# Kernel optimization log

Measured on AMD Instinct MI355X. Metric: run time of the kernel, lower is better.

Reference implementation:

```python
import jax, jax.numpy as jnp
from jax import lax
import numpy as np

EPS = 1e-07


def _sum_pool3_same(x):
    """TF avg_pool2d(3,1,'SAME')*9: sum over 3x3 window, edge windows scaled by 9/valid_count."""
    # x: [b, h, w, q]
    window = (1, 3, 3, 1)
    strides = (1, 1, 1, 1)
    s = lax.reduce_window(x, 0.0, lax.add, window, strides, 'SAME')
    ones = jnp.ones((1, x.shape[1], x.shape[2], 1), dtype=x.dtype)
    cnt = lax.reduce_window(ones, 0.0, lax.add, window, strides, 'SAME')
    return s / cnt * 9.0


def setup_inputs() -> dict:
    key = jax.random.key(0)
    k1, k2 = jax.random.split(key)
    foreground = jax.random.normal(k1, (4, 64, 64, 256), dtype=jnp.float32)
    masks = jax.random.uniform(k2, (4, 256, 256, 1), dtype=jnp.float32)
    return {"foreground": foreground, "masks": masks}


def reference(foreground, masks):
    # foreground: [bz, h, w, nc]; first-call forward (att_scores_prev is None).
    bz, h, w, nc = foreground.shape
    # masks resized to feature resolution (stored as state in original; no effect on output)
    if masks.shape[1] != h:
        masks = jax.image.resize(masks, (bz, h, w, masks.shape[-1]), method='bilinear')

    # 1x1 dynamic conv kernels from the feature map itself: K[b, q, c], q = flattened (h*w)
    K = (foreground + EPS).reshape(bz, h * w, nc)
    norm = jnp.sqrt(jnp.sum(K * K, axis=-1, keepdims=True))  # L2 norm per output channel q
    K = K / norm

    # conv2d with 1x1 kernels == per-pixel inner product with every patch center
    scores = jnp.einsum('bijc,bqc->bijq', foreground, K)  # [bz, h, w, h*w]

    # propagate_size=3: 3x3 smoothing (avg_pool * 9, TF edge-count semantics)
    scores = _sum_pool3_same(scores)

    att = jax.nn.softmax(scores, axis=-1)  # softmax over the h*w patch axis

    # conv2d_transpose with the same 1x1 kernels == weighted sum of patch features
    out = jnp.einsum('bijq,bqc->bijc', att, K)  # [bz, h, w, nc]
    return out
```

## Files before the change

### kernel.cpp

```cpp
#include <hip/hip_runtime.h>


#define EPSV 1e-7f

typedef __bf16 bf16x8 __attribute__((ext_vector_type(8)));
typedef float f32x4 __attribute__((ext_vector_type(4)));
typedef unsigned short ushort8v __attribute__((ext_vector_type(8)));

__device__ __forceinline__ unsigned short f2bf(float f) {
    union { float f; unsigned int u; } x; x.f = f;
    unsigned int r = x.u + 0x7FFFu + ((x.u >> 16) & 1u);
    return (unsigned short)(r >> 16);
}

__device__ __forceinline__ f32x4 mfma16(bf16x8 a, bf16x8 b, f32x4 c) {
    return __builtin_amdgcn_mfma_f32_16x16x32_bf16(a, b, c, 0, 0, 0);
}

__device__ __forceinline__ void gload_lds16(const void* g, void* l) {
    __builtin_amdgcn_global_load_lds((const __attribute__((address_space(1))) void*)g,
                                     (__attribute__((address_space(3))) void*)l, 16, 0, 0);
}

__global__ __launch_bounds__(256) void prep_kv(const float* __restrict__ F,
                                               unsigned short* __restrict__ Khi2,
                                               unsigned short* __restrict__ Vt2) {
    __shared__ unsigned short ldsT[256 * 74];
    __shared__ unsigned short ldsR[64 * 264];
    const int tid = threadIdx.x;
    const int w = tid >> 6, lane = tid & 63;
    const int q0 = blockIdx.x * 64;
    const int b = blockIdx.y;
    const size_t bq = (size_t)b * 4096;

    for (int r = 0; r < 16; ++r) {
        const int qloc = w * 16 + r;
        const int q = q0 + qloc;
        const float4 f = *(const float4*)(F + ((bq + q) << 8) + lane * 4);
        float v0 = f.x + EPSV, v1 = f.y + EPSV, v2 = f.z + EPSV, v3 = f.w + EPSV;
        float ss = v0 * v0 + v1 * v1 + v2 * v2 + v3 * v3;
        #pragma unroll
        for (int m = 1; m <= 32; m <<= 1) ss += __shfl_xor(ss, m);
        const float inv = 1.0f / sqrtf(ss);
        const unsigned short k0 = f2bf(v0 * inv), k1 = f2bf(v1 * inv);
        const unsigned short k2 = f2bf(v2 * inv), k3 = f2bf(v3 * inv);
        ushort4 kk; kk.x = k0; kk.y = k1; kk.z = k2; kk.w = k3;
        *(ushort4*)(ldsR + qloc * 264 + lane * 4) = kk;
        ldsT[(lane * 4 + 0) * 74 + qloc] = k0;
        ldsT[(lane * 4 + 1) * 74 + qloc] = k1;
        ldsT[(lane * 4 + 2) * 74 + qloc] = k2;
        ldsT[(lane * 4 + 3) * 74 + qloc] = k3;
    }
    __syncthreads();

    const size_t tbase = (size_t)b * 128 + (size_t)blockIdx.x * 2;

    #pragma unroll
    for (int tsub = 0; tsub < 2; ++tsub) {
        char* dstK = (char*)Khi2 + ((tbase + tsub) << 14);
        #pragma unroll
        for (int i = 0; i < 4; ++i) {
            const int fi = i * 256 + tid;
            const int chunk = fi >> 6, L = fi & 63;
            const int l15 = L & 15, g4v = L >> 4;
            const int kg = chunk >> 1, ct = chunk & 1;
            const int qloc = tsub * 32 + ct * 16 + l15;
            const int c0 = kg * 32 + g4v * 8;
            *(ushort8v*)(dstK + fi * 16) = *(const ushort8v*)(ldsR + qloc * 264 + c0);
        }
    }

    const int c = tid;
    const int c16v = c >> 4, l15c = c & 15;
    const unsigned short* row = ldsT + c * 74;
    #pragma unroll
    for (int tsub = 0; tsub < 2; ++tsub) {
        const unsigned short* qrow = row + tsub * 32;
        #pragma unroll
        for (int g4v = 0; g4v < 4; ++g4v) {
            ushort8v frag;
            #pragma unroll
            for (int e = 0; e < 8; ++e)
                frag[e] = qrow[(g4v * 4 + (e >> 1)) + ((e & 1) << 4)];
            *(ushort8v*)((char*)Vt2 + ((tbase + tsub) << 14) + (c16v << 10) +
                         ((g4v * 16 + l15c) << 4)) = frag;
        }
    }
}

__global__ __launch_bounds__(256) void prep_g(const float* __restrict__ F,
                                              unsigned short* __restrict__ G) {
    __shared__ float vs[64 * 256];
    const int tid = threadIdx.x;
    const int i = blockIdx.x, b = blockIdx.y;
    const size_t bq = (size_t)b * 4096;
    const int i0 = i > 0 ? i - 1 : 0, i1 = i < 63 ? i + 1 : 63;
    #pragma unroll
    for (int k2 = 0; k2 < 16; ++k2) {
        const int cell = k2 * 256 + tid;
        const int j = cell >> 6, c4 = (cell & 63) << 2;
        float4 acc = {0.f, 0.f, 0.f, 0.f};
        for (int ii = i0; ii <= i1; ++ii) {
            const float4 f = *(const float4*)(F + ((bq + ii * 64 + j) << 8) + c4);
            acc.x += f.x; acc.y += f.y; acc.z += f.z; acc.w += f.w;
        }
        *(float4*)(vs + j * 256 + c4) = acc;
    }
    __syncthreads();
    const float ri = (float)(i1 - i0 + 1);
    #pragma unroll
    for (int k2 = 0; k2 < 16; ++k2) {
        const int cell = k2 * 256 + tid;
        const int j = cell >> 6, c4 = (cell & 63) << 2;
        const int j0 = j > 0 ? j - 1 : 0, j1 = j < 63 ? j + 1 : 63;
        float4 s = {0.f, 0.f, 0.f, 0.f};
        for (int jj = j0; jj <= j1; ++jj) {
            const float4 v = *(const float4*)(vs + jj * 256 + c4);
            s.x += v.x; s.y += v.y; s.z += v.z; s.w += v.w;
        }
        const float scale = 9.0f / (ri * (float)(j1 - j0 + 1));
        ushort4 gv; gv.x = f2bf(s.x * scale); gv.y = f2bf(s.y * scale);
        gv.z = f2bf(s.z * scale); gv.w = f2bf(s.w * scale);
        *(ushort4*)(G + ((bq + i * 64 + j) << 8) + c4) = gv;
    }
}

template <int ATOMIC>
__global__ __launch_bounds__(256, 2) void attn_main(
        const unsigned short* __restrict__ Khi2, const unsigned short* __restrict__ Vt2,
        const unsigned short* __restrict__ G, float* __restrict__ wsl,
        float* __restrict__ dOut, float* __restrict__ wsO) {
    __shared__ unsigned short ldsK[2][32 * 256];
    __shared__ unsigned short ldsV[2][32 * 256];
    __shared__ unsigned int ldsP[4][32 * 20];
    const int tid = threadIdx.x;
    const int w = tid >> 6, lane = tid & 63;
    const int l15 = lane & 15, g4 = lane >> 4;

    const int bid = blockIdx.x;
    const int u = bid & 7, v = bid >> 3;
    const int group = u * 2 + (v >> 5);
    const int pb = v & 31;
    const int split = group >> 2, b = group & 3;

    const int pw = pb * 128 + w * 32;
    const size_t bq = (size_t)b * 4096;

    const char* KhiB = (const char*)Khi2 + (((size_t)b * 128 + split * 32) << 14);
    const char* VtB = (const char*)Vt2 + (((size_t)b * 128 + split * 32) << 14);

    #pragma unroll
    for (int it = 0; it < 4; ++it) {
        const int g = it * 256 + tid;
        gload_lds16(KhiB + g * 16, (char*)&ldsK[0][0] + g * 16);
    }
    #pragma unroll
    for (int it = 0; it < 4; ++it) {
        const int g = it * 256 + tid;
        gload_lds16(VtB + g * 16, (char*)&ldsV[0][0] + g * 16);
    }

    bf16x8 a[2][8];
    #pragma unroll
    for (int rt = 0; rt < 2; ++rt)
        #pragma unroll
        for (int kg = 0; kg < 8; ++kg)
            a[rt][kg] = *(const bf16x8*)(G + ((bq + pw + rt * 16 + l15) << 8) + (kg << 5) + (g4 << 3));

    f32x4 o[2][16];
    float lacc[2][4];
    #pragma unroll
    for (int rt = 0; rt < 2; ++rt) {
        #pragma unroll
        for (int c16 = 0; c16 < 16; ++c16) o[rt][c16] = f32x4{0.f, 0.f, 0.f, 0.f};
        #pragma unroll
        for (int r = 0; r < 4; ++r) lacc[rt][r] = 0.f;
    }
    unsigned int* Pw = &ldsP[w][0];

    __syncthreads();

    #pragma unroll 1
    for (int t = 0; t < 32; ++t) {
        const int cur = t & 1;

        if (t < 31) {
            const char* ks = KhiB + ((size_t)(t + 1) << 14);
            #pragma unroll
            for (int it = 0; it < 4; ++it) {
                const int g = it * 256 + tid;
                gload_lds16(ks + g * 16, (char*)&ldsK[cur ^ 1][0] + g * 16);
            }
            const char* vs2 = VtB + ((size_t)(t + 1) << 14);
            #pragma unroll
            for (int it = 0; it < 4; ++it) {
                const int g = it * 256 + tid;
                gload_lds16(vs2 + g * 16, (char*)&ldsV[cur ^ 1][0] + g * 16);
            }
        }

        f32x4 s[2][2];
        #pragma unroll
        for (int rt = 0; rt < 2; ++rt) {
            s[rt][0] = f32x4{0.f, 0.f, 0.f, 0.f};
            s[rt][1] = f32x4{0.f, 0.f, 0.f, 0.f};
        }
        const char* kb = (const char*)&ldsK[cur][0] + (lane << 4);
        __builtin_amdgcn_s_setprio(1);
        #pragma unroll
        for (int kg = 0; kg < 8; ++kg) {
            #pragma unroll
            for (int ct = 0; ct < 2; ++ct) {
                const bf16x8 bk = *(const bf16x8*)(kb + (kg * 2 + ct) * 1024);
                s[0][ct] = mfma16(a[0][kg], bk, s[0][ct]);
                s[1][ct] = mfma16(a[1][kg], bk, s[1][ct]);
            }
        }
        __builtin_amdgcn_s_setprio(0);

        bf16x8 a2[2];
        #pragma unroll
        for (int rt = 0; rt < 2; ++rt) {
            #pragma unroll
            for (int r = 0; r < 4; ++r) {
                const float e0 = __expf(s[rt][0][r]);
                const float e1 = __expf(s[rt][1][r]);
                lacc[rt][r] += e0 + e1;
                union { __bf16 h[2]; unsigned int u; } pk;
                pk.h[0] = (__bf16)e0; pk.h[1] = (__bf16)e1;
                Pw[(rt * 16 + g4 * 4 + r) * 20 + l15] = pk.u;
            }
            a2[rt] = *(const bf16x8*)((const char*)Pw + (rt * 16 + l15) * 80 + (g4 << 4));
        }

        const char* vbase = (const char*)&ldsV[cur][0] + (lane << 4);
        __builtin_amdgcn_s_setprio(1);
        #pragma unroll
        for (int c16 = 0; c16 < 16; ++c16) {
            const bf16x8 bv = *(const bf16x8*)(vbase + c16 * 1024);
            o[0][c16] = mfma16(bv, a2[0], o[0][c16]);
            o[1][c16] = mfma16(bv, a2[1], o[1][c16]);
        }
        __builtin_amdgcn_s_setprio(0);

        if (t < 31) __syncthreads();
    }

    #pragma unroll
    for (int rt = 0; rt < 2; ++rt)
        #pragma unroll
        for (int r = 0; r < 4; ++r) {
            float vsum = lacc[rt][r];
            #pragma unroll
            for (int m = 1; m <= 8; m <<= 1) vsum += __shfl_xor(vsum, m);
            lacc[rt][r] = vsum;
        }
    if (l15 == 0) {
        #pragma unroll
        for (int rt = 0; rt < 2; ++rt)
            #pragma unroll
            for (int r = 0; r < 4; ++r)
                wsl[(size_t)split * 16384 + bq + pw + rt * 16 + g4 * 4 + r] = lacc[rt][r];
    }

    if (!ATOMIC) {
        float* dst = (split == 0) ? dOut : (wsO + (size_t)(split - 1) * 4194304);
        #pragma unroll
        for (int rt = 0; rt < 2; ++rt)
            #pragma unroll
            for (int c16 = 0; c16 < 16; ++c16)
                *(f32x4*)(dst + ((bq + pw + rt * 16 + l15) << 8) + c16 * 16 + (g4 << 2)) = o[rt][c16];
    } else {
        #pragma unroll
        for (int rt = 0; rt < 2; ++rt)
            #pragma unroll
            for (int c16 = 0; c16 < 16; ++c16)
                #pragma unroll
                for (int r = 0; r < 4; ++r) {
                    const size_t idx = ((bq + pw + rt * 16 + l15) << 8) + c16 * 16 + (g4 << 2) + r;
                    atomicAdd(&dOut[idx], o[rt][c16][r]);
                }
    }
}

__global__ __launch_bounds__(256) void reduce_fin(float* __restrict__ dOut,
                                                  const float* __restrict__ wsO,
                                                  const float* __restrict__ wsl) {
    const int i4 = blockIdx.x * 256 + threadIdx.x;
    const int row = i4 >> 6;
    const float l = wsl[row] + wsl[16384 + row] + wsl[32768 + row] + wsl[49152 + row];
    const float inv = 1.0f / l;
    float4 v = ((const float4*)dOut)[i4];
    const float4 a = ((const float4*)wsO)[i4];
    const float4 b = ((const float4*)(wsO + 4194304))[i4];
    const float4 c = ((const float4*)(wsO + 8388608))[i4];
    v.x = (v.x + a.x + b.x + c.x) * inv;
    v.y = (v.y + a.y + b.y + c.y) * inv;
    v.z = (v.z + a.z + b.z + c.z) * inv;
    v.w = (v.w + a.w + b.w + c.w) * inv;
    ((float4*)dOut)[i4] = v;
}

__global__ __launch_bounds__(256) void divide_fin(float* __restrict__ dOut,
                                                  const float* __restrict__ wsl) {
    const int i4 = blockIdx.x * 256 + threadIdx.x;
    const int row = i4 >> 6;
    const float l = wsl[row] + wsl[16384 + row] + wsl[32768 + row] + wsl[49152 + row];
    const float inv = 1.0f / l;
    float4 v = ((const float4*)dOut)[i4];
    v.x *= inv; v.y *= inv; v.z *= inv; v.w *= inv;
    ((float4*)dOut)[i4] = v;
}

extern "C" void kernel_launch(void* const* d_in, const int* in_sizes, int n_in,
                              void* d_out, int out_size, void* d_ws, size_t ws_size,
                              hipStream_t stream) {
    const float* F = (const float*)d_in[0];
    float* out = (float*)d_out;
    char* ws = (char*)d_ws;

    unsigned short* Khi2 = (unsigned short*)ws;
    unsigned short* Vt2 = Khi2 + 4194304;
    unsigned short* G = Vt2 + 4194304;
    float* wsl = (float*)(ws + 25165824);
    float* wsO = (float*)(ws + 25165824 + 262144);
    const size_t needA = 25165824u + 262144u + 3u * 16777216u;

    prep_kv<<<dim3(64, 4), 256, 0, stream>>>(F, Khi2, Vt2);
    prep_g<<<dim3(64, 4), 256, 0, stream>>>(F, G);

    if (ws_size >= needA) {
        attn_main<0><<<dim3(512), 256, 0, stream>>>(Khi2, Vt2, G, wsl, out, wsO);
        reduce_fin<<<4096, 256, 0, stream>>>(out, wsO, wsl);
    } else {
        hipMemsetAsync(out, 0, 16777216, stream);
        attn_main<1><<<dim3(512), 256, 0, stream>>>(Khi2, Vt2, G, wsl, out, nullptr);
        divide_fin<<<4096, 256, 0, stream>>>(out, wsl);
    }
}
```

Before: 126.0 us.

## Restructure attention kernel to 512-thread blocks with 64-key tiles and shared P

The attention kernel now uses 8 waves per block and processes 64-key tiles instead of 32. Each wave computes scores for 64 rows against a 16-key slice and writes exp values to a swizzled shared P buffer. For the PV product, each wave covers a 64-channel slice across all keys, so V fragments are reused over four row tiles. The softmax denominator is now computed with an MFMA against a ones vector rather than shuffle reductions. Prep_kv writes the K/V images in the new 64-key tile layout, and an extra block-wide barrier per tile is added to share P.

```diff
diff --git a/kernel.cpp b/kernel.cpp
--- a/kernel.cpp
+++ b/kernel.cpp
@@ -23,8 +23,8 @@
 }
 
 __global__ __launch_bounds__(256) void prep_kv(const float* __restrict__ F,
-                                               unsigned short* __restrict__ Khi2,
-                                               unsigned short* __restrict__ Vt2) {
+                                               unsigned short* __restrict__ Kimg,
+                                               unsigned short* __restrict__ Vimg) {
     __shared__ unsigned short ldsT[256 * 74];
     __shared__ unsigned short ldsR[64 * 264];
     const int tid = threadIdx.x;
@@ -53,39 +53,31 @@
     }
     __syncthreads();
 
-    const size_t tbase = (size_t)b * 128 + (size_t)blockIdx.x * 2;
-
-    #pragma unroll
-    for (int tsub = 0; tsub < 2; ++tsub) {
-        char* dstK = (char*)Khi2 + ((tbase + tsub) << 14);
-        #pragma unroll
-        for (int i = 0; i < 4; ++i) {
-            const int fi = i * 256 + tid;
-            const int chunk = fi >> 6, L = fi & 63;
-            const int l15 = L & 15, g4v = L >> 4;
-            const int kg = chunk >> 1, ct = chunk & 1;
-            const int qloc = tsub * 32 + ct * 16 + l15;
-            const int c0 = kg * 32 + g4v * 8;
-            *(ushort8v*)(dstK + fi * 16) = *(const ushort8v*)(ldsR + qloc * 264 + c0);
-        }
-    }
-
-    const int c = tid;
-    const int c16v = c >> 4, l15c = c & 15;
-    const unsigned short* row = ldsT + c * 74;
-    #pragma unroll
-    for (int tsub = 0; tsub < 2; ++tsub) {
-        const unsigned short* qrow = row + tsub * 32;
+    const size_t tb = (((size_t)b * 64 + blockIdx.x) << 15);
+
+    #pragma unroll
+    for (int i = 0; i < 8; ++i) {
+        const int fi = i * 256 + tid;
+        const int chunk = fi >> 6, L = fi & 63;
+        const int kg = chunk >> 2, ct = chunk & 3;
+        const int qloc = ct * 16 + (L & 15);
+        const int c0 = kg * 32 + (L >> 4) * 8;
+        *(ushort8v*)((char*)Kimg + tb + fi * 16) = *(const ushort8v*)(ldsR + qloc * 264 + c0);
+    }
+
+    const int c16v = tid >> 4, l15c = tid & 15;
+    const unsigned short* row = ldsT + tid * 74;
+    #pragma unroll
+    for (int kq = 0; kq < 2; ++kq)
         #pragma unroll
         for (int g4v = 0; g4v < 4; ++g4v) {
             ushort8v frag;
             #pragma unroll
             for (int e = 0; e < 8; ++e)
-                frag[e] = qrow[(g4v * 4 + (e >> 1)) + ((e & 1) << 4)];
-            *(ushort8v*)((char*)Vt2 + ((tbase + tsub) << 14) + (c16v << 10) +
+                frag[e] = row[kq * 32 + g4v * 4 + (e >> 1) + ((e & 1) << 4)];
+            *(ushort8v*)((char*)Vimg + tb + (((c16v << 1) + kq) << 10) +
                          ((g4v * 16 + l15c) << 4)) = frag;
         }
-    }
 }
 
 __global__ __launch_bounds__(256) void prep_g(const float* __restrict__ F,
@@ -126,16 +118,18 @@
 }
 
 template <int ATOMIC>
-__global__ __launch_bounds__(256, 2) void attn_main(
-        const unsigned short* __restrict__ Khi2, const unsigned short* __restrict__ Vt2,
+__global__ __launch_bounds__(512, 2) void attn_main(
+        const unsigned short* __restrict__ Kimg, const unsigned short* __restrict__ Vimg,
         const unsigned short* __restrict__ G, float* __restrict__ wsl,
         float* __restrict__ dOut, float* __restrict__ wsO) {
-    __shared__ unsigned short ldsK[2][32 * 256];
-    __shared__ unsigned short ldsV[2][32 * 256];
-    __shared__ unsigned int ldsP[4][32 * 20];
+    __shared__ unsigned short ldsK[2][16384];
+    __shared__ unsigned short ldsV[2][16384];
+    __shared__ unsigned short ldsP[8192];
     const int tid = threadIdx.x;
     const int w = tid >> 6, lane = tid & 63;
     const int l15 = lane & 15, g4 = lane >> 4;
+    const int ph = w >> 2, qg = w & 3;
+    const int cg = w & 3;
 
     const int bid = blockIdx.x;
     const int u = bid & 7, v = bid >> 3;
@@ -143,142 +137,142 @@
     const int pb = v & 31;
     const int split = group >> 2, b = group & 3;
 
-    const int pw = pb * 128 + w * 32;
     const size_t bq = (size_t)b * 4096;
-
-    const char* KhiB = (const char*)Khi2 + (((size_t)b * 128 + split * 32) << 14);
-    const char* VtB = (const char*)Vt2 + (((size_t)b * 128 + split * 32) << 14);
+    const int pwave = pb * 128 + ph * 64;
+
+    const char* KimgB = (const char*)Kimg + (((size_t)b * 64 + split * 16) << 15);
+    const char* VimgB = (const char*)Vimg + (((size_t)b * 64 + split * 16) << 15);
 
     #pragma unroll
     for (int it = 0; it < 4; ++it) {
-        const int g = it * 256 + tid;
-        gload_lds16(KhiB + g * 16, (char*)&ldsK[0][0] + g * 16);
+        const int g = it * 512 + tid;
+        gload_lds16(KimgB + g * 16, (char*)&ldsK[0][0] + g * 16);
     }
     #pragma unroll
     for (int it = 0; it < 4; ++it) {
-        const int g = it * 256 + tid;
-        gload_lds16(VtB + g * 16, (char*)&ldsV[0][0] + g * 16);
-    }
-
-    bf16x8 a[2][8];
-    #pragma unroll
-    for (int rt = 0; rt < 2; ++rt)
+        const int g = it * 512 + tid;
+        gload_lds16(VimgB + g * 16, (char*)&ldsV[0][0] + g * 16);
+    }
+
+    bf16x8 a[4][8];
+    #pragma unroll
+    for (int rt = 0; rt < 4; ++rt)
         #pragma unroll
         for (int kg = 0; kg < 8; ++kg)
-            a[rt][kg] = *(const bf16x8*)(G + ((bq + pw + rt * 16 + l15) << 8) + (kg << 5) + (g4 << 3));
-
-    f32x4 o[2][16];
-    float lacc[2][4];
-    #pragma unroll
-    for (int rt = 0; rt < 2; ++rt) {
-        #pragma unroll
-        for (int c16 = 0; c16 < 16; ++c16) o[rt][c16] = f32x4{0.f, 0.f, 0.f, 0.f};
-        #pragma unroll
-        for (int r = 0; r < 4; ++r) lacc[rt][r] = 0.f;
-    }
-    unsigned int* Pw = &ldsP[w][0];
+            a[rt][kg] = *(const bf16x8*)(G + ((bq + pwave + rt * 16 + l15) << 8) + (kg << 5) + (g4 << 3));
+
+    f32x4 o[4][4];
+    f32x4 ol[4];
+    #pragma unroll
+    for (int i = 0; i < 4; ++i) {
+        #pragma unroll
+        for (int j = 0; j < 4; ++j) o[i][j] = f32x4{0.f, 0.f, 0.f, 0.f};
+        ol[i] = f32x4{0.f, 0.f, 0.f, 0.f};
+    }
+    bf16x8 ones;
+    #pragma unroll
+    for (int e = 0; e < 8; ++e) ones[e] = (__bf16)1.0f;
+
+    const int gx = ((l15 >> 2) & 3) << 1;
+    const int ebyte = ((l15 & 3) * 2 + (qg & 1)) * 2;
+    const int Lsw = lane ^ ((lane >> 4) << 1);
 
     __syncthreads();
 
     #pragma unroll 1
-    for (int t = 0; t < 32; ++t) {
+    for (int t = 0; t < 16; ++t) {
         const int cur = t & 1;
 
-        if (t < 31) {
-            const char* ks = KhiB + ((size_t)(t + 1) << 14);
+        if (t < 15) {
+            const char* ks = KimgB + ((size_t)(t + 1) << 15);
             #pragma unroll
             for (int it = 0; it < 4; ++it) {
-                const int g = it * 256 + tid;
+                const int g = it * 512 + tid;
                 gload_lds16(ks + g * 16, (char*)&ldsK[cur ^ 1][0] + g * 16);
             }
-            const char* vs2 = VtB + ((size_t)(t + 1) << 14);
+            const char* vsrc = VimgB + ((size_t)(t + 1) << 15);
             #pragma unroll
             for (int it = 0; it < 4; ++it) {
-                const int g = it * 256 + tid;
-                gload_lds16(vs2 + g * 16, (char*)&ldsV[cur ^ 1][0] + g * 16);
-            }
-        }
-
-        f32x4 s[2][2];
-        #pragma unroll
-        for (int rt = 0; rt < 2; ++rt) {
-            s[rt][0] = f32x4{0.f, 0.f, 0.f, 0.f};
-            s[rt][1] = f32x4{0.f, 0.f, 0.f, 0.f};
-        }
-        const char* kb = (const char*)&ldsK[cur][0] + (lane << 4);
+                const int g = it * 512 + tid;
+                gload_lds16(vsrc + g * 16, (char*)&ldsV[cur ^ 1][0] + g * 16);
+            }
+        }
+
+        f32x4 s[4];
+        #pragma unroll
+        for (int rt = 0; rt < 4; ++rt) s[rt] = f32x4{0.f, 0.f, 0.f, 0.f};
+        const char* kb = (const char*)&ldsK[cur][0] + (qg << 10) + (lane << 4);
         __builtin_amdgcn_s_setprio(1);
         #pragma unroll
         for (int kg = 0; kg < 8; ++kg) {
-            #pragma unroll
-            for (int ct = 0; ct < 2; ++ct) {
-                const bf16x8 bk = *(const bf16x8*)(kb + (kg * 2 + ct) * 1024);
-                s[0][ct] = mfma16(a[0][kg], bk, s[0][ct]);
-                s[1][ct] = mfma16(a[1][kg], bk, s[1][ct]);
-            }
+            const bf16x8 bk = *(const bf16x8*)(kb + (kg << 12));
+            #pragma unroll
+            for (int rt = 0; rt < 4; ++rt) s[rt] = mfma16(a[rt][kg], bk, s[rt]);
         }
         __builtin_amdgcn_s_setprio(0);
 
-        bf16x8 a2[2];
-        #pragma unroll
-        for (int rt = 0; rt < 2; ++rt) {
+        #pragma unroll
+        for (int rt = 0; rt < 4; ++rt) {
+            char* pw = (char*)ldsP + ((((ph * 4 + rt) << 1) + (qg >> 1)) << 10);
             #pragma unroll
             for (int r = 0; r < 4; ++r) {
-                const float e0 = __expf(s[rt][0][r]);
-                const float e1 = __expf(s[rt][1][r]);
-                lacc[rt][r] += e0 + e1;
-                union { __bf16 h[2]; unsigned int u; } pk;
-                pk.h[0] = (__bf16)e0; pk.h[1] = (__bf16)e1;
-                Pw[(rt * 16 + g4 * 4 + r) * 20 + l15] = pk.u;
-            }
-            a2[rt] = *(const bf16x8*)((const char*)Pw + (rt * 16 + l15) * 80 + (g4 << 4));
-        }
-
-        const char* vbase = (const char*)&ldsV[cur][0] + (lane << 4);
+                const float e = __expf(s[rt][r]);
+                const int gsw = ((l15 >> 2) * 16 + g4 * 4 + r) ^ gx;
+                union { __bf16 h; unsigned short us; } cv; cv.h = (__bf16)e;
+                *(unsigned short*)(pw + gsw * 16 + ebyte) = cv.us;
+            }
+        }
+
+        __syncthreads();
+
         __builtin_amdgcn_s_setprio(1);
         #pragma unroll
-        for (int c16 = 0; c16 < 16; ++c16) {
-            const bf16x8 bv = *(const bf16x8*)(vbase + c16 * 1024);
-            o[0][c16] = mfma16(bv, a2[0], o[0][c16]);
-            o[1][c16] = mfma16(bv, a2[1], o[1][c16]);
+        for (int kq = 0; kq < 2; ++kq) {
+            bf16x8 pa[4];
+            #pragma unroll
+            for (int j = 0; j < 4; ++j)
+                pa[j] = *(const bf16x8*)((const char*)ldsP +
+                            ((((ph * 4 + j) << 1) + kq) << 10) + Lsw * 16);
+            #pragma unroll
+            for (int i = 0; i < 4; ++i) {
+                const bf16x8 bv = *(const bf16x8*)((const char*)&ldsV[cur][0] +
+                                    ((((cg * 4 + i) << 1) + kq) << 10) + (lane << 4));
+                #pragma unroll
+                for (int j = 0; j < 4; ++j) o[i][j] = mfma16(bv, pa[j], o[i][j]);
+            }
+            if (cg == 0) {
+                #pragma unroll
+                for (int j = 0; j < 4; ++j) ol[j] = mfma16(ones, pa[j], ol[j]);
+            }
         }
         __builtin_amdgcn_s_setprio(0);
 
-        if (t < 31) __syncthreads();
-    }
-
-    #pragma unroll
-    for (int rt = 0; rt < 2; ++rt)
-        #pragma unroll
-        for (int r = 0; r < 4; ++r) {
-            float vsum = lacc[rt][r];
-            #pragma unroll
-            for (int m = 1; m <= 8; m <<= 1) vsum += __shfl_xor(vsum, m);
-            lacc[rt][r] = vsum;
-        }
-    if (l15 == 0) {
-        #pragma unroll
-        for (int rt = 0; rt < 2; ++rt)
-            #pragma unroll
-            for (int r = 0; r < 4; ++r)
-                wsl[(size_t)split * 16384 + bq + pw + rt * 16 + g4 * 4 + r] = lacc[rt][r];
-    }
-
+        __syncthreads();
+    }
+
+    if (cg == 0 && g4 == 0) {
+        #pragma unroll
+        for (int j = 0; j < 4; ++j)
+            wsl[(size_t)split * 16384 + bq + pb * 128 + ph * 64 + j * 16 + l15] = ol[j][0];
+    }
     if (!ATOMIC) {
         float* dst = (split == 0) ? dOut : (wsO + (size_t)(split - 1) * 4194304);
         #pragma unroll
-        for (int rt = 0; rt < 2; ++rt)
-            #pragma unroll
-            for (int c16 = 0; c16 < 16; ++c16)
-                *(f32x4*)(dst + ((bq + pw + rt * 16 + l15) << 8) + c16 * 16 + (g4 << 2)) = o[rt][c16];
+        for (int i = 0; i < 4; ++i)
+            #pragma unroll
+            for (int j = 0; j < 4; ++j)
+                *(f32x4*)(dst + ((bq + pb * 128 + ph * 64 + j * 16 + l15) << 8) +
+                          cg * 64 + i * 16 + (g4 << 2)) = o[i][j];
     } else {
         #pragma unroll
-        for (int rt = 0; rt < 2; ++rt)
-            #pragma unroll
-            for (int c16 = 0; c16 < 16; ++c16)
+        for (int i = 0; i < 4; ++i)
+            #pragma unroll
+            for (int j = 0; j < 4; ++j)
                 #pragma unroll
                 for (int r = 0; r < 4; ++r) {
-                    const size_t idx = ((bq + pw + rt * 16 + l15) << 8) + c16 * 16 + (g4 << 2) + r;
-                    atomicAdd(&dOut[idx], o[rt][c16][r]);
+                    const size_t idx = ((bq + pb * 128 + ph * 64 + j * 16 + l15) << 8) +
+                                       cg * 64 + i * 16 + (g4 << 2) + r;
+                    atomicAdd(&dOut[idx], o[i][j][r]);
                 }
     }
 }
@@ -319,22 +313,22 @@
     float* out = (float*)d_out;
     char* ws = (char*)d_ws;
 
-    unsigned short* Khi2 = (unsigned short*)ws;
-    unsigned short* Vt2 = Khi2 + 4194304;
-    unsigned short* G = Vt2 + 4194304;
+    unsigned short* Kimg = (unsigned short*)ws;
+    unsigned short* Vimg = Kimg + 4194304;
+    unsigned short* G = Vimg + 4194304;
     float* wsl = (float*)(ws + 25165824);
     float* wsO = (float*)(ws + 25165824 + 262144);
     const size_t needA = 25165824u + 262144u + 3u * 16777216u;
 
-    prep_kv<<<dim3(64, 4), 256, 0, stream>>>(F, Khi2, Vt2);
+    prep_kv<<<dim3(64, 4), 256, 0, stream>>>(F, Kimg, Vimg);
     prep_g<<<dim3(64, 4), 256, 0, stream>>>(F, G);
 
     if (ws_size >= needA) {
-        attn_main<0><<<dim3(512), 256, 0, stream>>>(Khi2, Vt2, G, wsl, out, wsO);
+        attn_main<0><<<dim3(512), 512, 0, stream>>>(Kimg, Vimg, G, wsl, out, wsO);
         reduce_fin<<<4096, 256, 0, stream>>>(out, wsO, wsl);
     } else {
         hipMemsetAsync(out, 0, 16777216, stream);
-        attn_main<1><<<dim3(512), 256, 0, stream>>>(Khi2, Vt2, G, wsl, out, nullptr);
+        attn_main<1><<<dim3(512), 512, 0, stream>>>(Kimg, Vimg, G, wsl, out, nullptr);
         divide_fin<<<4096, 256, 0, stream>>>(out, wsl);
     }
 }
```

Result: slower. 146.5 us, median of 3 (+16.3%).
